# Kernel tuning notes

Hardware: AMD Instinct MI355X
Metric: run time of the kernel (lower is better)

The kernel has to match this reference:

```python
import jax, jax.numpy as jnp
import numpy as np

N = 4096      # nodes (= attention seq_len)
D = 256       # dim_h
H = 4         # num_heads
HD = D // H   # head dim
E = 131072    # edges (avg degree 32)


def _ln(x, g, b, eps=1e-5):
    mu = jnp.mean(x, -1, keepdims=True)
    var = jnp.var(x, -1, keepdims=True)
    return (x - mu) * jax.lax.rsqrt(var + eps) * g + b


def setup_inputs() -> dict:
    key = jax.random.key(0)
    ks = jax.random.split(key, 10)
    s = 0.02
    nrm = lambda k, shape: jax.random.normal(k, shape, jnp.float32) * s
    return dict(
        x=jax.random.normal(ks[0], (N, D), jnp.float32),
        edge_index=jax.random.randint(ks[1], (2, E), 0, N, dtype=jnp.int32),
        W_gcn=nrm(ks[2], (D, D)), b_gcn=jnp.zeros((D,), jnp.float32),
        w_qkv=nrm(ks[3], (D, 3 * D)), b_qkv=jnp.zeros((3 * D,), jnp.float32),
        w_out=nrm(ks[4], (D, D)), b_out=jnp.zeros((D,), jnp.float32),
        g1l=jnp.ones((D,), jnp.float32), beta1l=jnp.zeros((D,), jnp.float32),
        g1a=jnp.ones((D,), jnp.float32), beta1a=jnp.zeros((D,), jnp.float32),
        W1=nrm(ks[5], (D, 2 * D)), bf1=jnp.zeros((2 * D,), jnp.float32),
        W2=nrm(ks[6], (2 * D, D)), bf2=jnp.zeros((D,), jnp.float32),
        g2=jnp.ones((D,), jnp.float32), beta2=jnp.zeros((D,), jnp.float32),
    )


def reference(x, edge_index, W_gcn, b_gcn, w_qkv, b_qkv, w_out, b_out,
              g1l, beta1l, g1a, beta1a, W1, bf1, W2, bf2, g2, beta2):
    n = x.shape[0]
    # --- GCNConv: sym-normalized aggregation with self loops ---
    loop = jnp.arange(n, dtype=edge_index.dtype)
    src = jnp.concatenate([edge_index[0], loop])
    dst = jnp.concatenate([edge_index[1], loop])
    deg = jax.ops.segment_sum(jnp.ones_like(src, x.dtype), dst, num_segments=n)
    dinv = jax.lax.rsqrt(deg)  # deg >= 1 thanks to self loops
    h = x @ W_gcn                                  # [N, D]
    msg = h[src] * (dinv[src] * dinv[dst])[:, None]  # gather + edge norm
    x_local = jax.ops.segment_sum(msg, dst, num_segments=n) + b_gcn
    x = _ln(x + x_local, g1l, beta1l)
    # --- Multi-head self-attention over all nodes (one sequence) ---
    qkv = x @ w_qkv + b_qkv
    q, k, v = jnp.split(qkv, 3, axis=-1)
    q = q.reshape(n, H, HD)
    k = k.reshape(n, H, HD)
    v = v.reshape(n, H, HD)
    scale = 1.0 / (HD ** 0.5)
    scores = jnp.einsum('nhd,mhd->hnm', q, k) * scale   # [H, N, N]
    attn = jax.nn.softmax(scores, axis=-1)
    x_attn = jnp.einsum('hnm,mhd->nhd', attn, v).reshape(n, D) @ w_out + b_out
    x = _ln(x + x_attn, g1a, beta1a)
    # --- FFN (D -> 2D -> D, ReLU) ---
    x_ffn = jax.nn.relu(x @ W1 + bf1) @ W2 + bf2
    return _ln(x + x_ffn, g2, beta2)
```

## Files before the change

### kernel.cpp

```cpp
#include <hip/hip_runtime.h>

typedef unsigned short u16;
typedef __bf16 bf16x8 __attribute__((ext_vector_type(8)));
typedef float f32x4 __attribute__((ext_vector_type(4)));
typedef float f32x16 __attribute__((ext_vector_type(16)));
typedef unsigned u32x4v __attribute__((ext_vector_type(4)));

__device__ __forceinline__ u16 f2u(float f) {
    unsigned u = __builtin_bit_cast(unsigned, f);
    return (u16)((u + 0x7FFFu + ((u >> 16) & 1u)) >> 16);
}

__device__ __forceinline__ float u2f(u16 h) {
    return __builtin_bit_cast(float, (unsigned)h << 16);
}

__device__ __forceinline__ void glds16(const u16* g, u16* l) {
    __builtin_amdgcn_global_load_lds((const __attribute__((address_space(1))) unsigned int*)g,
                                     (__attribute__((address_space(3))) unsigned int*)l, 16, 0, 0);
}


__global__ __launch_bounds__(256) void prep_k(
    const float* __restrict__ w0, const float* __restrict__ w1, const float* __restrict__ w2,
    const float* __restrict__ w3, const float* __restrict__ w4, const float* __restrict__ x,
    u16* __restrict__ o0, u16* __restrict__ o1, u16* __restrict__ o2,
    u16* __restrict__ o3, u16* __restrict__ o4, u16* __restrict__ xo,
    int* __restrict__ cnt, int xblocks, int nn) {
    int b = blockIdx.x, t = threadIdx.x;
    if (b < 144) {
        const float* in; u16* out; int R, C, tb;
        if (b < 16)       { in = w0; out = o0; R = 256; C = 256; tb = b; }
        else if (b < 64)  { in = w1; out = o1; R = 256; C = 768; tb = b - 16; }
        else if (b < 80)  { in = w2; out = o2; R = 256; C = 256; tb = b - 64; }
        else if (b < 112) { in = w3; out = o3; R = 256; C = 512; tb = b - 80; }
        else              { in = w4; out = o4; R = 512; C = 256; tb = b - 112; }
        int tcols = C >> 6;
        int tr = tb / tcols, tc = tb - tr * tcols;
        __shared__ float T[64][65];
        int i0 = t >> 6, j = t & 63;
#pragma unroll
        for (int p = 0; p < 16; p++) {
            int r = p * 4 + i0;
            T[r][j] = in[(long)(tr * 64 + r) * C + tc * 64 + j];
        }
        __syncthreads();
#pragma unroll
        for (int p = 0; p < 16; p++) {
            int c = p * 4 + i0;
            out[(long)(tc * 64 + c) * R + tr * 64 + j] = f2u(T[j][c]);
        }
    } else if (b < 144 + xblocks) {
        long base = (long)(b - 144) * 4096;
#pragma unroll
        for (int p = 0; p < 4; p++) {
            long idx = base + p * 1024 + t * 4;
            float4 v = *(const float4*)&x[idx];
            unsigned lo = (unsigned)f2u(v.x) | ((unsigned)f2u(v.y) << 16);
            unsigned hi = (unsigned)f2u(v.z) | ((unsigned)f2u(v.w) << 16);
            *(uint2*)&xo[idx] = uint2{lo, hi};
        }
    } else {
        int i = (b - 144 - xblocks) * 256 + t;
        if (i < nn) cnt[i] = 0;
    }
}


__device__ __forceinline__ void block_ln_stats(float v, float& mu, float& rstd) {
    float s1 = v, s2 = v * v;
#pragma unroll
    for (int m = 1; m < 64; m <<= 1) { s1 += __shfl_xor(s1, m, 64); s2 += __shfl_xor(s2, m, 64); }
    __shared__ float r1[4], r2[4];
    int lane = threadIdx.x & 63, w = threadIdx.x >> 6;
    if (lane == 0) { r1[w] = s1; r2[w] = s2; }
    __syncthreads();
    s1 = r1[0] + r1[1] + r1[2] + r1[3];
    s2 = r2[0] + r2[1] + r2[2] + r2[3];
    mu = s1 * (1.0f / 256.0f);
    float var = s2 * (1.0f / 256.0f) - mu * mu;
    rstd = rsqrtf(var + 1e-5f);
}


__global__ __launch_bounds__(256) void gcn_agg_ln_k(
    const u16* __restrict__ h, const float* __restrict__ x,
    const int* __restrict__ srcs, const int* __restrict__ cnt,
    const float* __restrict__ bg,
    const float* __restrict__ g, const float* __restrict__ be,
    float* __restrict__ x1, u16* __restrict__ x1bf) {
    int n = blockIdx.x, d = threadIdx.x;
    int c = cnt[n]; c = c < 128 ? c : 128;
    int st = n << 7;
    float dn = rsqrtf((float)(c + 1));
    float agg = u2f(h[(long)n * 256 + d]) * dn;
    int e = 0;
    for (; e + 4 <= c; e += 4) {
        int s0 = srcs[st + e], s1 = srcs[st + e + 1], s2 = srcs[st + e + 2], s3 = srcs[st + e + 3];
        float a0 = u2f(h[(long)s0 * 256 + d]) * rsqrtf((float)(cnt[s0] + 1));
        float a1 = u2f(h[(long)s1 * 256 + d]) * rsqrtf((float)(cnt[s1] + 1));
        float a2 = u2f(h[(long)s2 * 256 + d]) * rsqrtf((float)(cnt[s2] + 1));
        float a3 = u2f(h[(long)s3 * 256 + d]) * rsqrtf((float)(cnt[s3] + 1));
        agg += (a0 + a1) + (a2 + a3);
    }
    for (; e < c; e++) {
        int s = srcs[st + e];
        agg += u2f(h[(long)s * 256 + d]) * rsqrtf((float)(cnt[s] + 1));
    }
    float v = x[(long)n * 256 + d] + dn * agg + bg[d];
    float mu, rs;
    block_ln_stats(v, mu, rs);
    float y = (v - mu) * rs * g[d] + be[d];
    x1[(long)n * 256 + d] = y;
    x1bf[(long)n * 256 + d] = f2u(y);
}


template <int EPI>
__device__ __forceinline__ void gemm_body(
    int bx, int by,
    const u16* __restrict__ A, const u16* __restrict__ Bt,
    const float* __restrict__ bias, void* __restrict__ outp,
    int M, int N, int K) {
    __shared__ __align__(16) u16 As[64 * 256];
    __shared__ __align__(16) u16 Bs[64 * 256];
    int tid = threadIdx.x;
    int lane = tid & 63, w = tid >> 6;
    int l15 = lane & 15, quad = lane >> 4, l7 = l15 & 7;
    int m0 = bx * 64, n0 = by * 64;
    int wm = (w >> 1) * 32, wn = (w & 1) * 32;
    f32x4 acc[2][2];
#pragma unroll
    for (int i = 0; i < 2; i++)
#pragma unroll
        for (int j = 0; j < 2; j++) acc[i][j] = f32x4{0.f, 0.f, 0.f, 0.f};

    int rA0 = (wm + l15) * 256, rA1 = (wm + 16 + l15) * 256;
    int rB0 = (wn + l15) * 256, rB1 = (wn + 16 + l15) * 256;

    for (int kb = 0; kb < K; kb += 256) {
        if (kb) __syncthreads();
#pragma unroll
        for (int i = 0; i < 8; i++) {
            int s = i * 256 + tid;
            int j = s >> 5, dch = s & 31;
            int c = dch ^ (j & 7);
            glds16(A + (long)(m0 + j) * K + kb + c * 8, &As[s * 8]);
            glds16(Bt + (long)(n0 + j) * K + kb + c * 8, &Bs[s * 8]);
        }
        __syncthreads();
#pragma unroll
        for (int step = 0; step < 8; step++) {
            int d8 = (((step << 2) + quad) ^ l7) << 3;
            bf16x8 af0 = *(const bf16x8*)&As[rA0 + d8];
            bf16x8 af1 = *(const bf16x8*)&As[rA1 + d8];
            bf16x8 bf0 = *(const bf16x8*)&Bs[rB0 + d8];
            bf16x8 bf1 = *(const bf16x8*)&Bs[rB1 + d8];
            acc[0][0] = __builtin_amdgcn_mfma_f32_16x16x32_bf16(af0, bf0, acc[0][0], 0, 0, 0);
            acc[0][1] = __builtin_amdgcn_mfma_f32_16x16x32_bf16(af0, bf1, acc[0][1], 0, 0, 0);
            acc[1][0] = __builtin_amdgcn_mfma_f32_16x16x32_bf16(af1, bf0, acc[1][0], 0, 0, 0);
            acc[1][1] = __builtin_amdgcn_mfma_f32_16x16x32_bf16(af1, bf1, acc[1][1], 0, 0, 0);
        }
    }

#pragma unroll
    for (int nf = 0; nf < 2; nf++) {
        int col = n0 + wn + nf * 16 + l15;
        float bv = bias ? bias[col] : 0.0f;
#pragma unroll
        for (int mf = 0; mf < 2; mf++) {
#pragma unroll
            for (int r = 0; r < 4; r++) {
                int row = m0 + wm + mf * 16 + quad * 4 + r;
                float v = acc[mf][nf][r] + bv;
                if (EPI == 1) {
                    u16* q = (u16*)outp;
                    u16* kk = q + (long)M * 256;
                    u16* vt = kk + (long)M * 256;
                    if (col < 256) {
                        q[(((col >> 6) * (long)M) + row) * 64 + (col & 63)] = f2u(v * 0.180336884f);
                    } else if (col < 512) {
                        int c = col - 256;
                        kk[(((c >> 6) * (long)M) + row) * 64 + (c & 63)] = f2u(v);
                    } else {
                        int c = col - 512;
                        vt[((c >> 6) * 64 + (c & 63)) * (long)M + row] = f2u(v);
                    }
                } else if (EPI == 2) {
                    ((u16*)outp)[(long)row * N + col] = f2u(v > 0.f ? v : 0.f);
                } else {
                    ((u16*)outp)[(long)row * N + col] = f2u(v);
                }
            }
        }
    }
}

template <int EPI>
__global__ __launch_bounds__(256) void gemm_k(
    const u16* __restrict__ A, const u16* __restrict__ Bt,
    const float* __restrict__ bias, void* __restrict__ outp,
    int M, int N, int K) {
    gemm_body<EPI>(blockIdx.x, blockIdx.y, A, Bt, bias, outp, M, N, K);
}


template <int WRITE_BF>
__global__ __launch_bounds__(256) void gemm_ln_k(
    const u16* __restrict__ A, const u16* __restrict__ Bt, const float* __restrict__ bias,
    const float* __restrict__ res, const float* __restrict__ g, const float* __restrict__ be,
    float* __restrict__ outf, u16* __restrict__ outbf, int M, int K) {
    __shared__ __align__(16) u16 As[16 * 64];
    __shared__ __align__(16) u16 Bs[256 * 64];
    __shared__ float red[2][4][16];
    int tid = threadIdx.x;
    int lane = tid & 63, w = tid >> 6;
    int l15 = lane & 15, quad = lane >> 4, l7 = l15 & 7;
    int m0 = blockIdx.x * 16;
    f32x4 acc[4];
#pragma unroll
    for (int i = 0; i < 4; i++) acc[i] = f32x4{0.f, 0.f, 0.f, 0.f};

    int jA = tid >> 3, dA = tid & 7, cA = dA ^ (jA & 7);
    const u16* agp = A + (long)(m0 + jA) * K + cA * 8;

    for (int kb = 0; kb < K; kb += 64) {
        if (kb) __syncthreads();
        if (tid < 128) glds16(agp + kb, &As[tid * 8]);
#pragma unroll
        for (int i = 0; i < 8; i++) {
            int s = i * 256 + tid;
            int jb = s >> 3, db = s & 7, cb = db ^ (jb & 7);
            glds16(Bt + (long)jb * K + kb + cb * 8, &Bs[s * 8]);
        }
        __syncthreads();
#pragma unroll
        for (int step = 0; step < 2; step++) {
            int d8 = (((step << 2) + quad) ^ l7) << 3;
            bf16x8 af = *(const bf16x8*)&As[l15 * 64 + d8];
#pragma unroll
            for (int nf = 0; nf < 4; nf++) {
                int rb = w * 64 + nf * 16 + l15;
                bf16x8 bfr = *(const bf16x8*)&Bs[rb * 64 + d8];
                acc[nf] = __builtin_amdgcn_mfma_f32_16x16x32_bf16(af, bfr, acc[nf], 0, 0, 0);
            }
        }
    }

    float vv[4][4];
    float p1[4] = {0.f, 0.f, 0.f, 0.f}, p2[4] = {0.f, 0.f, 0.f, 0.f};
#pragma unroll
    for (int nf = 0; nf < 4; nf++) {
        int col = w * 64 + nf * 16 + l15;
        float bv = bias[col];
#pragma unroll
        for (int r = 0; r < 4; r++) {
            int row = m0 + quad * 4 + r;
            float v = acc[nf][r] + bv + res[(long)row * 256 + col];
            vv[nf][r] = v;
            p1[r] += v; p2[r] += v * v;
        }
    }
#pragma unroll
    for (int m = 1; m < 16; m <<= 1) {
#pragma unroll
        for (int r = 0; r < 4; r++) {
            p1[r] += __shfl_xor(p1[r], m, 64);
            p2[r] += __shfl_xor(p2[r], m, 64);
        }
    }
    if (l15 == 0) {
#pragma unroll
        for (int r = 0; r < 4; r++) { red[0][w][quad * 4 + r] = p1[r]; red[1][w][quad * 4 + r] = p2[r]; }
    }
    __syncthreads();
    float mu[4], rs[4];
#pragma unroll
    for (int r = 0; r < 4; r++) {
        int rr = quad * 4 + r;
        float s1 = red[0][0][rr] + red[0][1][rr] + red[0][2][rr] + red[0][3][rr];
        float s2 = red[1][0][rr] + red[1][1][rr] + red[1][2][rr] + red[1][3][rr];
        mu[r] = s1 * (1.0f / 256.0f);
        float var = s2 * (1.0f / 256.0f) - mu[r] * mu[r];
        rs[r] = rsqrtf(var + 1e-5f);
    }
#pragma unroll
    for (int nf = 0; nf < 4; nf++) {
        int col = w * 64 + nf * 16 + l15;
        float gg = g[col], bb = be[col];
#pragma unroll
        for (int r = 0; r < 4; r++) {
            int row = m0 + quad * 4 + r;
            float y = (vv[nf][r] - mu[r]) * rs[r] * gg + bb;
            outf[(long)row * 256 + col] = y;
            if (WRITE_BF) outbf[(long)row * 256 + col] = f2u(y);
        }
    }
}


__global__ __launch_bounds__(256) void front_k(
    const int* __restrict__ ei, int E, int* __restrict__ cnt, int* __restrict__ srcs,
    const u16* __restrict__ A, const u16* __restrict__ Bt, void* __restrict__ outp,
    int M, int N, int K, int SB) {
    int b = blockIdx.x;
    if (b < SB) {
        int e = b * 256 + threadIdx.x;
        if (e < E) {
            int s = ei[e], d = ei[E + e];
            int p = atomicAdd(&cnt[d], 1);
            if (p < 128) srcs[(d << 7) + p] = s;
        }
    } else {
        int id = b - SB;
        gemm_body<3>(id & 63, id >> 6, A, Bt, nullptr, outp, M, N, K);
    }
}


__global__ __launch_bounds__(256) void attn_k(const u16* __restrict__ qg, const u16* __restrict__ kg,
                                              const u16* __restrict__ vtg, float* __restrict__ po,
                                              float* __restrict__ pl, int N, int S) {
    int tid = threadIdx.x;
    int w = tid >> 6, lane = tid & 63;
    int l31 = lane & 31, h = lane >> 5, xr = l31 & 7;
    int hh = blockIdx.y, sp = blockIdx.z;
    int q0w = blockIdx.x * 128 + w * 32;
    int kbeg = sp * (N / S);
    int nit = (N / S) / 64;
    const u16* qh = qg + (long)hh * N * 64;
    const u16* kh = kg + (long)hh * N * 64;
    const u16* vh = vtg + (long)hh * 64 * N;

    __shared__ __align__(16) u16 KV[2][2][4096];

    int s0 = tid, j0 = s0 >> 3, c0s = ((s0 & 7) ^ (j0 & 7)) * 8;
    int s1 = tid + 256, j1 = s1 >> 3, c1s = ((s1 & 7) ^ (j1 & 7)) * 8;
    const u16* kp0 = kh + (long)(kbeg + j0) * 64 + c0s;
    const u16* kp1 = kh + (long)(kbeg + j1) * 64 + c1s;
    const u16* vp0 = vh + (long)j0 * N + kbeg + c0s;
    const u16* vp1 = vh + (long)j1 * N + kbeg + c1s;
    u16* lk0[2] = {&KV[0][0][s0 * 8], &KV[1][0][s0 * 8]};
    u16* lk1[2] = {&KV[0][0][s1 * 8], &KV[1][0][s1 * 8]};
    u16* lv0[2] = {&KV[0][1][s0 * 8], &KV[1][1][s0 * 8]};
    u16* lv1[2] = {&KV[0][1][s1 * 8], &KV[1][1][s1 * 8]};

    bf16x8 qf[4];
#pragma unroll
    for (int stp = 0; stp < 4; stp++)
        qf[stp] = *(const bf16x8*)(qh + (long)(q0w + l31) * 64 + stp * 16 + h * 8);

    f32x16 o0{}, o1{};
    float ll = 0.f;

    glds16(kp0, lk0[0]); glds16(kp1, lk1[0]);
    glds16(vp0, lv0[0]); glds16(vp1, lv1[0]);
    kp0 += 4096; kp1 += 4096; vp0 += 64; vp1 += 64;

    for (int it = 0; it < nit; it++) {
        __syncthreads();
        if (it + 1 < nit) {
            int nb = (it + 1) & 1;
            glds16(kp0, lk0[nb]); glds16(kp1, lk1[nb]);
            glds16(vp0, lv0[nb]); glds16(vp1, lv1[nb]);
            kp0 += 4096; kp1 += 4096; vp0 += 64; vp1 += 64;
        }
        const u16* Kc = &KV[it & 1][0][0];
        const u16* Vc = &KV[it & 1][1][0];

        f32x16 sA{}, sB{};
#pragma unroll
        for (int stp = 0; stp < 4; stp++) {
            int cc = (((stp << 1) + h) ^ xr) * 8;
            bf16x8 kfa = *(const bf16x8*)&Kc[l31 * 64 + cc];
            bf16x8 kfb = *(const bf16x8*)&Kc[(32 + l31) * 64 + cc];
            sA = __builtin_amdgcn_mfma_f32_32x32x16_bf16(kfa, qf[stp], sA, 0, 0, 0);
            sB = __builtin_amdgcn_mfma_f32_32x32x16_bf16(kfb, qf[stp], sB, 0, 0, 0);
        }

#pragma unroll
        for (int kt = 0; kt < 2; kt++) {
            f32x16 s = kt ? sB : sA;
            unsigned wr[8];
#pragma unroll
            for (int i = 0; i < 8; i++) {
                unsigned ua = (unsigned)((int)(s[2 * i] * 8388608.0f) + 1064992209);
                unsigned ub = (unsigned)((int)(s[2 * i + 1] * 8388608.0f) + 1064992209);
                ll += __builtin_bit_cast(float, ua & 0xffff0000u);
                ll += __builtin_bit_cast(float, ub & 0xffff0000u);
                wr[i] = __builtin_amdgcn_perm(ub, ua, 0x07060302u);
            }
            asm("v_permlane32_swap_b32 %0, %1" : "+v"(wr[2]), "+v"(wr[0]));
            asm("v_permlane32_swap_b32 %0, %1" : "+v"(wr[3]), "+v"(wr[1]));
            asm("v_permlane32_swap_b32 %0, %1" : "+v"(wr[6]), "+v"(wr[4]));
            asm("v_permlane32_swap_b32 %0, %1" : "+v"(wr[7]), "+v"(wr[5]));
            u32x4v t0 = {wr[0], wr[1], wr[2], wr[3]};
            u32x4v t1 = {wr[4], wr[5], wr[6], wr[7]};
            bf16x8 f0 = __builtin_bit_cast(bf16x8, t0);
            bf16x8 f1 = __builtin_bit_cast(bf16x8, t1);

#pragma unroll
            for (int dt = 0; dt < 2; dt++) {
                int rowb = (dt * 32 + l31) * 64;
                bf16x8 v0 = *(const bf16x8*)&Vc[rowb + (((kt << 2) + h) ^ xr) * 8];
                bf16x8 v1 = *(const bf16x8*)&Vc[rowb + (((kt << 2) + 2 + h) ^ xr) * 8];
                if (dt == 0) {
                    o0 = __builtin_amdgcn_mfma_f32_32x32x16_bf16(f0, v0, o0, 0, 0, 0);
                    o0 = __builtin_amdgcn_mfma_f32_32x32x16_bf16(f1, v1, o0, 0, 0, 0);
                } else {
                    o1 = __builtin_amdgcn_mfma_f32_32x32x16_bf16(f0, v0, o1, 0, 0, 0);
                    o1 = __builtin_amdgcn_mfma_f32_32x32x16_bf16(f1, v1, o1, 0, 0, 0);
                }
            }
        }
    }

    ll += __shfl_xor(ll, 32, 64);
    long pbase = ((long)(sp * 4 + hh)) * N;
#pragma unroll
    for (int dt = 0; dt < 2; dt++)
#pragma unroll
        for (int r = 0; r < 16; r++) {
            int qrow = q0w + (r & 3) + ((r >> 2) << 3) + (h << 2);
            float val = dt ? o1[r] : o0[r];
            po[(pbase + qrow) * 64 + dt * 32 + l31] = val;
        }
    if (lane < 32) pl[pbase + q0w + lane] = ll;
}

__global__ __launch_bounds__(256) void attn_comb_k(const float* __restrict__ po, const float* __restrict__ pl,
                                                   u16* __restrict__ xo, int N, int S) {
    int n = blockIdx.x, c = threadIdx.x;
    int hh = c >> 6, d = c & 63;
    float osum = 0.f, lsum = 0.f;
    for (int s = 0; s < S; s++) {
        osum += po[(((long)(s * 4 + hh)) * N + n) * 64 + d];
        lsum += pl[((long)(s * 4 + hh)) * N + n];
    }
    xo[(long)n * 256 + c] = f2u(osum / lsum);
}


extern "C" void kernel_launch(void* const* d_in, const int* in_sizes, int n_in,
                              void* d_out, int out_size, void* d_ws, size_t ws_size,
                              hipStream_t stream) {
    const float* x    = (const float*)d_in[0];
    const int*   ei   = (const int*)d_in[1];
    const float* Wg   = (const float*)d_in[2];
    const float* bg   = (const float*)d_in[3];
    const float* Wqkv = (const float*)d_in[4];
    const float* bqkv = (const float*)d_in[5];
    const float* Wo   = (const float*)d_in[6];
    const float* bo   = (const float*)d_in[7];
    const float* g1l  = (const float*)d_in[8];
    const float* b1l  = (const float*)d_in[9];
    const float* g1a  = (const float*)d_in[10];
    const float* b1a  = (const float*)d_in[11];
    const float* W1   = (const float*)d_in[12];
    const float* bf1  = (const float*)d_in[13];
    const float* W2   = (const float*)d_in[14];
    const float* bf2  = (const float*)d_in[15];
    const float* g2   = (const float*)d_in[16];
    const float* b2   = (const float*)d_in[17];
    float* out = (float*)d_out;

    int N = in_sizes[0] / 256;
    int E = in_sizes[1] / 2;
    const int S = 4;

    char* p = (char*)d_ws;
    auto alloc = [&](size_t bytes) { void* r = (void*)p; p += (bytes + 255) & ~(size_t)255; return r; };
    u16*   wg_t   = (u16*)alloc((size_t)256 * 256 * 2);
    u16*   wqkv_t = (u16*)alloc((size_t)256 * 768 * 2);
    u16*   wo_t   = (u16*)alloc((size_t)256 * 256 * 2);
    u16*   w1_t   = (u16*)alloc((size_t)512 * 256 * 2);
    u16*   w2_t   = (u16*)alloc((size_t)256 * 512 * 2);
    u16*   xbf    = (u16*)alloc((size_t)N * 256 * 2);
    u16*   h      = (u16*)alloc((size_t)N * 256 * 2);
    int*   cnt    = (int*)alloc((size_t)N * 4);
    int*   srcs   = (int*)alloc((size_t)N * 128 * 4);
    float* x1     = (float*)alloc((size_t)N * 256 * 4);
    u16*   x1bf   = (u16*)alloc((size_t)N * 256 * 2);
    u16*   qkv    = (u16*)alloc((size_t)3 * N * 256 * 2);
    u16*   xattn  = (u16*)alloc((size_t)N * 256 * 2);
    float* x2     = (float*)alloc((size_t)N * 256 * 4);
    u16*   x2bf   = (u16*)alloc((size_t)N * 256 * 2);
    u16*   ffn1   = (u16*)alloc((size_t)N * 512 * 2);
    float* po     = (float*)alloc((size_t)S * 4 * N * 64 * 4);
    float* pl     = (float*)alloc((size_t)S * 4 * N * 4);

    dim3 b256(256);

    int xblocks = (N * 256) / 4096;
    int cblocks = (N + 255) / 256;
    prep_k<<<144 + xblocks + cblocks, b256, 0, stream>>>(Wg, Wqkv, Wo, W1, W2, x,
                                                         wg_t, wqkv_t, wo_t, w1_t, w2_t, xbf,
                                                         cnt, xblocks, N);

    int SB = (E + 255) / 256;
    front_k<<<SB + (N / 64) * 4, b256, 0, stream>>>(ei, E, cnt, srcs, xbf, wg_t, h, N, 256, 256, SB);

    gcn_agg_ln_k<<<N, b256, 0, stream>>>(h, x, srcs, cnt, bg, g1l, b1l, x1, x1bf);

    gemm_k<1><<<dim3(N / 64, 12), b256, 0, stream>>>(x1bf, wqkv_t, bqkv, qkv, N, 768, 256);
    attn_k<<<dim3(N / 128, 4, S), b256, 0, stream>>>(qkv, qkv + (size_t)N * 256, qkv + (size_t)2 * N * 256,
                                                     po, pl, N, S);
    attn_comb_k<<<N, b256, 0, stream>>>(po, pl, xattn, N, S);

    gemm_ln_k<1><<<N / 16, b256, 0, stream>>>(xattn, wo_t, bo, x1, g1a, b1a, x2, x2bf, N, 256);

    gemm_k<2><<<dim3(N / 64, 8), b256, 0, stream>>>(x2bf, w1_t, bf1, ffn1, N, 512, 256);

    gemm_ln_k<0><<<N / 16, b256, 0, stream>>>(ffn1, w2_t, bf2, x2, g2, b2, out, nullptr, N, 512);
}
```

Before: 187.2 us.

## Fuse attention split combine into out-proj GEMM+LN and compute row sums via MFMA

Removes the separate attn_comb_k launch by merging the split-K combine (summing partial outputs and dividing by partial denominators) into the output-projection GEMM + LayerNorm kernel, which now stages the combined bf16 A tile in LDS. This drops one kernel launch and the xattn round trip through global memory. In attention, the per-lane scalar accumulation of softmax denominators is replaced by extra MFMAs against a ones vector, moving that work from VALU to the matrix unit. The cost is extra MFMA work per tile and denominators summed from bf16-rounded probabilities rather than from the truncated fp32 values used before.

Measured after the change: 202.0 us. 1.08x slower.

```diff
diff --git a/kernel.cpp b/kernel.cpp
--- a/kernel.cpp
+++ b/kernel.cpp
@@ -299,6 +299,114 @@
 }
 
 
+__global__ __launch_bounds__(256) void comb_gemm_ln_k(
+    const float* __restrict__ po, const float* __restrict__ pl,
+    const u16* __restrict__ Bt, const float* __restrict__ bias,
+    const float* __restrict__ res, const float* __restrict__ g, const float* __restrict__ be,
+    float* __restrict__ outf, u16* __restrict__ outbf, int M, int S) {
+    const int K = 256;
+    __shared__ __align__(16) u16 As16[16 * 256];
+    __shared__ __align__(16) u16 Bs[256 * 64];
+    __shared__ float red[2][4][16];
+    int tid = threadIdx.x;
+    int lane = tid & 63, w = tid >> 6;
+    int l15 = lane & 15, quad = lane >> 4, l7 = l15 & 7;
+    int m0 = blockIdx.x * 16;
+
+    {
+        int d = lane;
+        int g8 = w * 8 + (d >> 3), e = d & 7;
+#pragma unroll
+        for (int r = 0; r < 16; r++) {
+            float osum = 0.f, lsum = 0.f;
+            for (int s = 0; s < S; s++) {
+                long pb = ((long)(s * 4 + w)) * M;
+                osum += po[(pb + m0 + r) * 64 + d];
+                lsum += pl[pb + m0 + r];
+            }
+            int slot = (g8 & ~7) | ((g8 & 7) ^ (r & 7));
+            As16[r * 256 + slot * 8 + e] = f2u(osum / lsum);
+        }
+    }
+
+    f32x4 acc[4];
+#pragma unroll
+    for (int i = 0; i < 4; i++) acc[i] = f32x4{0.f, 0.f, 0.f, 0.f};
+
+    for (int kb = 0; kb < K; kb += 64) {
+        if (kb) __syncthreads();
+#pragma unroll
+        for (int i = 0; i < 8; i++) {
+            int s = i * 256 + tid;
+            int jb = s >> 3, db = s & 7, cb = db ^ (jb & 7);
+            glds16(Bt + (long)jb * K + kb + cb * 8, &Bs[s * 8]);
+        }
+        __syncthreads();
+#pragma unroll
+        for (int step = 0; step < 2; step++) {
+            int d8 = (((step << 2) + quad) ^ l7) << 3;
+            bf16x8 af = *(const bf16x8*)&As16[l15 * 256 + kb + d8];
+#pragma unroll
+            for (int nf = 0; nf < 4; nf++) {
+                int rb = w * 64 + nf * 16 + l15;
+                bf16x8 bfr = *(const bf16x8*)&Bs[rb * 64 + d8];
+                acc[nf] = __builtin_amdgcn_mfma_f32_16x16x32_bf16(af, bfr, acc[nf], 0, 0, 0);
+            }
+        }
+    }
+
+    float vv[4][4];
+    float p1[4] = {0.f, 0.f, 0.f, 0.f}, p2[4] = {0.f, 0.f, 0.f, 0.f};
+#pragma unroll
+    for (int nf = 0; nf < 4; nf++) {
+        int col = w * 64 + nf * 16 + l15;
+        float bv = bias[col];
+#pragma unroll
+        for (int r = 0; r < 4; r++) {
+            int row = m0 + quad * 4 + r;
+            float v = acc[nf][r] + bv + res[(long)row * 256 + col];
+            vv[nf][r] = v;
+            p1[r] += v; p2[r] += v * v;
+        }
+    }
+#pragma unroll
+    for (int m = 1; m < 16; m <<= 1) {
+#pragma unroll
+        for (int r = 0; r < 4; r++) {
+            p1[r] += __shfl_xor(p1[r], m, 64);
+            p2[r] += __shfl_xor(p2[r], m, 64);
+        }
+    }
+    if (l15 == 0) {
+#pragma unroll
+        for (int r = 0; r < 4; r++) { red[0][w][quad * 4 + r] = p1[r]; red[1][w][quad * 4 + r] = p2[r]; }
+    }
+    __syncthreads();
+    float mu[4], rs[4];
+#pragma unroll
+    for (int r = 0; r < 4; r++) {
+        int rr = quad * 4 + r;
+        float s1 = red[0][0][rr] + red[0][1][rr] + red[0][2][rr] + red[0][3][rr];
+        float s2 = red[1][0][rr] + red[1][1][rr] + red[1][2][rr] + red[1][3][rr];
+        mu[r] = s1 * (1.0f / 256.0f);
+        float var = s2 * (1.0f / 256.0f) - mu[r] * mu[r];
+        rs[r] = rsqrtf(var + 1e-5f);
+    }
+#pragma unroll
+    for (int nf = 0; nf < 4; nf++) {
+        int col = w * 64 + nf * 16 + l15;
+        float gg = g[col], bb = be[col];
+#pragma unroll
+        for (int r = 0; r < 4; r++) {
+            int row = m0 + quad * 4 + r;
+            float y = (vv[nf][r] - mu[r]) * rs[r] * gg + bb;
+            outf[(long)row * 256 + col] = y;
+            outbf[(long)row * 256 + col] = f2u(y);
+        }
+    }
+}
+
+
 __global__ __launch_bounds__(256) void front_k(
     const int* __restrict__ ei, int E, int* __restrict__ cnt, int* __restrict__ srcs,
     const u16* __restrict__ A, const u16* __restrict__ Bt, void* __restrict__ outp,
@@ -350,8 +458,11 @@
     for (int stp = 0; stp < 4; stp++)
         qf[stp] = *(const bf16x8*)(qh + (long)(q0w + l31) * 64 + stp * 16 + h * 8);
 
-    f32x16 o0{}, o1{};
-    float ll = 0.f;
+    bf16x8 ones;
+#pragma unroll
+    for (int i = 0; i < 8; i++) ones[i] = (__bf16)1.0f;
+
+    f32x16 o0{}, o1{}, accl{};
 
     glds16(kp0, lk0[0]); glds16(kp1, lk1[0]);
     glds16(vp0, lv0[0]); glds16(vp1, lv1[0]);
@@ -386,8 +497,6 @@
             for (int i = 0; i < 8; i++) {
                 unsigned ua = (unsigned)((int)(s[2 * i] * 8388608.0f) + 1064992209);
                 unsigned ub = (unsigned)((int)(s[2 * i + 1] * 8388608.0f) + 1064992209);
-                ll += __builtin_bit_cast(float, ua & 0xffff0000u);
-                ll += __builtin_bit_cast(float, ub & 0xffff0000u);
                 wr[i] = __builtin_amdgcn_perm(ub, ua, 0x07060302u);
             }
             asm("v_permlane32_swap_b32 %0, %1" : "+v"(wr[2]), "+v"(wr[0]));
@@ -398,6 +507,9 @@
             u32x4v t1 = {wr[4], wr[5], wr[6], wr[7]};
             bf16x8 f0 = __builtin_bit_cast(bf16x8, t0);
             bf16x8 f1 = __builtin_bit_cast(bf16x8, t1);
+
+            accl = __builtin_amdgcn_mfma_f32_32x32x16_bf16(f0, ones, accl, 0, 0, 0);
+            accl = __builtin_amdgcn_mfma_f32_32x32x16_bf16(f1, ones, accl, 0, 0, 0);
 
 #pragma unroll
             for (int dt = 0; dt < 2; dt++) {
@@ -415,7 +527,6 @@
         }
     }
 
-    ll += __shfl_xor(ll, 32, 64);
     long pbase = ((long)(sp * 4 + hh)) * N;
 #pragma unroll
     for (int dt = 0; dt < 2; dt++)
@@ -425,19 +536,13 @@
             float val = dt ? o1[r] : o0[r];
             po[(pbase + qrow) * 64 + dt * 32 + l31] = val;
         }
-    if (lane < 32) pl[pbase + q0w + lane] = ll;
-}
-
-__global__ __launch_bounds__(256) void attn_comb_k(const float* __restrict__ po, const float* __restrict__ pl,
-                                                   u16* __restrict__ xo, int N, int S) {
-    int n = blockIdx.x, c = threadIdx.x;
-    int hh = c >> 6, d = c & 63;
-    float osum = 0.f, lsum = 0.f;
-    for (int s = 0; s < S; s++) {
-        osum += po[(((long)(s * 4 + hh)) * N + n) * 64 + d];
-        lsum += pl[((long)(s * 4 + hh)) * N + n];
-    }
-    xo[(long)n * 256 + c] = f2u(osum / lsum);
+    if (l31 == 0) {
+#pragma unroll
+        for (int r = 0; r < 16; r++) {
+            int qrow = q0w + (r & 3) + ((r >> 2) << 3) + (h << 2);
+            pl[pbase + qrow] = accl[r];
+        }
+    }
 }
 
 
@@ -482,7 +587,6 @@
     float* x1     = (float*)alloc((size_t)N * 256 * 4);
     u16*   x1bf   = (u16*)alloc((size_t)N * 256 * 2);
     u16*   qkv    = (u16*)alloc((size_t)3 * N * 256 * 2);
-    u16*   xattn  = (u16*)alloc((size_t)N * 256 * 2);
     float* x2     = (float*)alloc((size_t)N * 256 * 4);
     u16*   x2bf   = (u16*)alloc((size_t)N * 256 * 2);
     u16*   ffn1   = (u16*)alloc((size_t)N * 512 * 2);
@@ -505,9 +609,8 @@
     gemm_k<1><<<dim3(N / 64, 12), b256, 0, stream>>>(x1bf, wqkv_t, bqkv, qkv, N, 768, 256);
     attn_k<<<dim3(N / 128, 4, S), b256, 0, stream>>>(qkv, qkv + (size_t)N * 256, qkv + (size_t)2 * N * 256,
                                                      po, pl, N, S);
-    attn_comb_k<<<N, b256, 0, stream>>>(po, pl, xattn, N, S);
-
-    gemm_ln_k<1><<<N / 16, b256, 0, stream>>>(xattn, wo_t, bo, x1, g1a, b1a, x2, x2bf, N, 256);
+
+    comb_gemm_ln_k<<<N / 16, b256, 0, stream>>>(po, pl, wo_t, bo, x1, g1a, b1a, x2, x2bf, N, S);
 
     gemm_k<2><<<dim3(N / 64, 8), b256, 0, stream>>>(x2bf, w1_t, bf1, ffn1, N, 512, 256);
 
```
